# Kernel optimization log

Measured on AMD Instinct MI355X. Metric: run time of the kernel, lower is better.

The kernel has to match this reference:

```python
import jax, jax.numpy as jnp
import numpy as np

# ---- dims (match init_kwargs / input_specs) ----
N = 50000        # nodes
E = 600000       # edges
F_IN = 128       # n_features
HID = 128        # hidden_dims
K = 8            # heads
D_A = 16         # attention dim per head
D_V = 16         # value dim per head
D_M = 64         # max-pool gate dim
CLASSES = 40     # n_classes
LAYERS = 2
SLOPE = 0.1      # negative_slop


def glorot(key, shape):
    lim = jnp.sqrt(6.0 / (shape[-2] + shape[-1]))
    return jax.random.uniform(key, shape, minval=-lim, maxval=lim, dtype=jnp.float32)


def setup_inputs() -> dict:
    key = jax.random.key(0)
    ks = jax.random.split(key, 10)
    x = jax.random.normal(ks[0], (N, F_IN), dtype=jnp.float32)
    edge_index = jax.random.randint(ks[1], (2, E), 0, N, dtype=jnp.int64)
    weight_in = glorot(ks[2], (F_IN, HID))
    weight_out = glorot(ks[3], (HID, CLASSES))
    # per-layer GaANConv params, stacked on leading layer dim
    Wq = glorot(ks[4], (LAYERS, HID, K * D_A))            # query proj
    Wk = glorot(ks[5], (LAYERS, HID, K * D_A))            # key proj
    Wv = glorot(ks[6], (LAYERS, HID, K * D_V))            # value proj
    Wm = glorot(ks[7], (LAYERS, HID, D_M))                # max-pool gate proj
    Wg = glorot(ks[8], (LAYERS, HID + D_M + HID, K))      # gate FC
    Wo = glorot(ks[9], (LAYERS, HID + K * D_V, HID))      # output proj
    return {"x": x, "edge_index": edge_index, "weight_in": weight_in,
            "weight_out": weight_out, "Wq": Wq, "Wk": Wk, "Wv": Wv,
            "Wm": Wm, "Wg": Wg, "Wo": Wo}


def gaan_conv(x, src, dst, wq, wk, wv, wm, wg, wo):
    n = x.shape[0]
    q = (x @ wq).reshape(n, K, D_A)
    k = (x @ wk).reshape(n, K, D_A)
    v = (x @ wv).reshape(n, K, D_V)
    # dot-product attention logits per edge/head: <q_dst, k_src>
    score = jnp.einsum('ekd,ekd->ek', q[dst], k[src])          # [E,K]
    # segment softmax over incoming edges of each dst node
    smax = jax.ops.segment_max(score, dst, num_segments=n)     # [N,K]
    smax = jnp.where(jnp.isfinite(smax), smax, 0.0)            # empty segments -> 0
    ex = jnp.exp(score - smax[dst])
    denom = jax.ops.segment_sum(ex, dst, num_segments=n)
    alpha = ex / (denom[dst] + 1e-16)                          # [E,K]
    agg = jax.ops.segment_sum(alpha[:, :, None] * v[src], dst, num_segments=n)  # [N,K,D_V]
    # gates: sigmoid(FC([x_i, max_j FC_m(x_j), mean_j x_j]))
    m = x @ wm                                                 # [N,D_M]
    maxpool = jax.ops.segment_max(m[src], dst, num_segments=n)
    maxpool = jnp.where(jnp.isfinite(maxpool), maxpool, 0.0)
    deg = jax.ops.segment_sum(jnp.ones((src.shape[0],), x.dtype), dst, num_segments=n)
    meanpool = jax.ops.segment_sum(x[src], dst, num_segments=n) / jnp.maximum(deg, 1.0)[:, None]
    g = jax.nn.sigmoid(jnp.concatenate([x, maxpool, meanpool], axis=1) @ wg)  # [N,K]
    gated = (g[:, :, None] * agg).reshape(n, K * D_V)
    return jnp.concatenate([x, gated], axis=1) @ wo            # [N,HID]


def reference(x, edge_index, weight_in, weight_out, Wq, Wk, Wv, Wm, Wg, Wo):
    src, dst = edge_index[0], edge_index[1]
    h = x @ weight_in
    for i in range(LAYERS):
        h = jax.nn.leaky_relu(
            gaan_conv(h, src, dst, Wq[i], Wk[i], Wv[i], Wm[i], Wg[i], Wo[i]),
            negative_slope=SLOPE)
        # dropout is identity in eval mode
    out = h @ weight_out
    return jax.nn.log_softmax(out, axis=1)
```

## Files before the change

kernel.cpp:

```cpp
#include <hip/hip_runtime.h>
#include <math.h>

#define NNODES 50000
#define NEDGES 600000
#define HIDDIM 128
#define NHEAD 8
#define DM 64
#define NCLS 40
#define FSTR 584
#define OFF_K 128
#define OFF_V 256
#define OFF_M 384
#define OFF_HG 448
#define OFF_H 456

typedef __attribute__((ext_vector_type(8))) short short8;
typedef __attribute__((ext_vector_type(4))) float f32x4;

static __device__ __forceinline__ unsigned short f2bf(float f) {
    unsigned u = __float_as_uint(f);
    unsigned r = (u + 0x7fffu + ((u >> 16) & 1u)) >> 16;
    return (unsigned short)r;
}
static __device__ __forceinline__ float bflo(unsigned u) { return __uint_as_float(u << 16); }
static __device__ __forceinline__ float bfhi(unsigned u) { return __uint_as_float(u & 0xffff0000u); }
static __device__ __forceinline__ float bf2f(unsigned short s) {
    return __uint_as_float(((unsigned)s) << 16);
}

template <int WF32, int WB1, int ACT>
__global__ __launch_bounds__(256) void gemm_mfma(
    const unsigned short* __restrict__ A1, int lda1, int K1,
    const unsigned short* __restrict__ A2, int lda2, int K2,
    const unsigned short* __restrict__ BT,
    float* __restrict__ C, int ldc,
    unsigned short* __restrict__ Cb1, int ldb1, int off1,
    int M, int NN)
{
    const int K = K1 + K2;
    const int l = threadIdx.x & 63, wv = threadIdx.x >> 6;
    const int r = l & 15, g = l >> 4;
    const int row0 = blockIdx.y * 128 + wv * 32;
    const int col0 = blockIdx.x * 64;

    f32x4 acc[2][4] = {};

    for (int k0 = 0; k0 < K; k0 += 32) {
        const unsigned short* Ak;
        int ka, lda;
        if (k0 < K1) { Ak = A1; ka = k0; lda = lda1; }
        else         { Ak = A2; ka = k0 - K1; lda = lda2; }

        short8 a[2], b[4];
#pragma unroll
        for (int m = 0; m < 2; ++m) {
            int row = row0 + m * 16 + r;
            if (row < M)
                a[m] = *reinterpret_cast<const short8*>(Ak + (size_t)row * lda + ka + 8 * g);
            else
                a[m] = short8{0, 0, 0, 0, 0, 0, 0, 0};
        }
#pragma unroll
        for (int n = 0; n < 4; ++n) {
            int col = col0 + n * 16 + r;
            b[n] = *reinterpret_cast<const short8*>(BT + (size_t)col * K + k0 + 8 * g);
        }
#pragma unroll
        for (int m = 0; m < 2; ++m)
#pragma unroll
            for (int n = 0; n < 4; ++n)
                acc[m][n] = __builtin_amdgcn_mfma_f32_16x16x32_bf16(a[m], b[n], acc[m][n], 0, 0, 0);
    }

#pragma unroll
    for (int m = 0; m < 2; ++m) {
#pragma unroll
        for (int j = 0; j < 4; ++j) {
            int row = row0 + m * 16 + 4 * g + j;
            if (row >= M) continue;
#pragma unroll
            for (int n = 0; n < 4; ++n) {
                int col = col0 + n * 16 + r;
                if (col >= NN) continue;
                float vv = acc[m][n][j];
                if (ACT) vv = vv > 0.f ? vv : 0.1f * vv;
                if (WF32) C[(size_t)row * ldc + col] = vv;
                if (WB1)  Cb1[(size_t)row * ldb1 + off1 + col] = f2bf(vv);
            }
        }
    }
}

#define BT_TOTAL 206848
__global__ __launch_bounds__(256) void pack_weights(
    const float* __restrict__ w_in, const float* __restrict__ w_out,
    const float* __restrict__ Wq, const float* __restrict__ Wk,
    const float* __restrict__ Wv, const float* __restrict__ Wm,
    const float* __restrict__ Wg, const float* __restrict__ Wo,
    unsigned short* __restrict__ BT)
{
    int i = blockIdx.x * 256 + threadIdx.x;
    if (i >= BT_TOTAL) return;
    float val;
    if (i < 16384) {
        int c = i >> 7, k = i & 127;
        val = w_in[k * 128 + c];
    } else if (i < 133120) {
        int li = i - 16384;
        int L = li / 58368, t = li % 58368;
        int c = t >> 7, k = t & 127;
        if      (c < 128) val = Wq[L * 16384 + k * 128 + c];
        else if (c < 256) val = Wk[L * 16384 + k * 128 + (c - 128)];
        else if (c < 384) val = Wv[L * 16384 + k * 128 + (c - 256)];
        else if (c < 448) val = Wm[L * 8192  + k * 64  + (c - 384)];
        else              val = Wg[L * 2560 + (192 + k) * 8 + (c - 448)];
    } else if (i < 198656) {
        int li = i - 133120;
        int L = li / 32768, t = li % 32768;
        int c = t >> 8, k = t & 255;
        val = Wo[L * 32768 + k * 128 + c];
    } else {
        int t = i - 198656;
        int c = t >> 7, k = t & 127;
        val = (c < NCLS) ? w_out[k * NCLS + c] : 0.f;
    }
    BT[i] = f2bf(val);
}

__global__ __launch_bounds__(256) void convert_x_kernel(
    const float* __restrict__ x, unsigned int* __restrict__ xb2)
{
    int i = blockIdx.x * 256 + threadIdx.x;
    if (i >= NNODES * HIDDIM / 2) return;
    float2 f = *reinterpret_cast<const float2*>(x + (size_t)i * 2);
    xb2[i] = (unsigned)f2bf(f.x) | ((unsigned)f2bf(f.y) << 16);
}

__global__ __launch_bounds__(256) void hist_kernel(
    const int* __restrict__ ei, int* __restrict__ degi)
{
    int e = blockIdx.x * 256 + threadIdx.x;
    if (e >= NEDGES) return;
    unsigned d = (unsigned)ei[NEDGES + e]; if (d >= NNODES) d = 0;
    atomicAdd(&degi[d], 1);
}

__global__ __launch_bounds__(1024) void scan_kernel(
    const int* __restrict__ degi, int* __restrict__ rowptr)
{
    __shared__ int sh[1024];
    const int t = threadIdx.x;
    const int chunk = (NNODES + 1023) / 1024;
    int lo = t * chunk, hi = min(lo + chunk, NNODES);
    int s = 0;
    for (int i = lo; i < hi; ++i) s += degi[i];
    sh[t] = s;
    __syncthreads();
    for (int off = 1; off < 1024; off <<= 1) {
        int v = (t >= off) ? sh[t - off] : 0;
        __syncthreads();
        sh[t] += v;
        __syncthreads();
    }
    int excl = (t == 0) ? 0 : sh[t - 1];
    for (int i = lo; i < hi; ++i) {
        rowptr[i] = excl;
        excl += degi[i];
    }
    if (t == 1023) rowptr[NNODES] = excl;
}

__global__ __launch_bounds__(256) void scatter_kernel(
    const int* __restrict__ ei, const int* __restrict__ rowptr,
    int* __restrict__ fill, int* __restrict__ csr_src)
{
    int e = blockIdx.x * 256 + threadIdx.x;
    if (e >= NEDGES) return;
    unsigned s = (unsigned)ei[e];          if (s >= NNODES) s = 0;
    unsigned d = (unsigned)ei[NEDGES + e]; if (d >= NNODES) d = 0;
    int pos = rowptr[d] + atomicAdd(&fill[d], 1);
    csr_src[pos] = (int)s;
}

__global__ __launch_bounds__(256) void fused_edge_kernel(
    const int* __restrict__ rowptr, const int* __restrict__ csr_src,
    const unsigned short* __restrict__ feat, const float* __restrict__ Wg,
    unsigned short* __restrict__ gatedb)
{
    int node = blockIdx.x * 4 + (threadIdx.x >> 6);
    if (node >= NNODES) return;
    const int lane = threadIdx.x & 63;
    const int c2 = lane * 2;
    const int j0 = lane & 7;

    const int start = rowptr[node], end = rowptr[node + 1];
    const int deg = end - start;

    const unsigned short* frow = feat + (size_t)node * FSTR;
    unsigned qu = *reinterpret_cast<const unsigned*>(frow + c2);
    float qx = bflo(qu), qy = bfhi(qu);

    float mr = -INFINITY, dr = 0.f;
    float a0 = 0.f, a1 = 0.f;
    float hgs = 0.f;
    float mm = -INFINITY;

    int p = start;
    for (; p + 2 <= end; p += 2) {
        int s0 = csr_src[p], s1 = csr_src[p + 1];
        const unsigned short* r0 = feat + (size_t)s0 * FSTR;
        const unsigned short* r1 = feat + (size_t)s1 * FSTR;
        unsigned ku0 = *reinterpret_cast<const unsigned*>(r0 + OFF_K + c2);
        unsigned vu0 = *reinterpret_cast<const unsigned*>(r0 + OFF_V + c2);
        float    mv0 = bf2f(r0[OFF_M + lane]);
        float    hg0 = bf2f(r0[OFF_HG + j0]);
        unsigned ku1 = *reinterpret_cast<const unsigned*>(r1 + OFF_K + c2);
        unsigned vu1 = *reinterpret_cast<const unsigned*>(r1 + OFF_V + c2);
        float    mv1 = bf2f(r1[OFF_M + lane]);
        float    hg1 = bf2f(r1[OFF_HG + j0]);

        float sc0 = qx * bflo(ku0) + qy * bfhi(ku0);
        float sc1 = qx * bflo(ku1) + qy * bfhi(ku1);
        sc0 += __shfl_xor(sc0, 1);  sc1 += __shfl_xor(sc1, 1);
        sc0 += __shfl_xor(sc0, 2);  sc1 += __shfl_xor(sc1, 2);
        sc0 += __shfl_xor(sc0, 4);  sc1 += __shfl_xor(sc1, 4);

        float nm = fmaxf(mr, fmaxf(sc0, sc1));
        float scale = __expf(mr - nm);
        float e0 = __expf(sc0 - nm), e1 = __expf(sc1 - nm);
        dr = dr * scale + e0 + e1;
        a0 = a0 * scale; a0 = fmaf(e0, bflo(vu0), a0); a0 = fmaf(e1, bflo(vu1), a0);
        a1 = a1 * scale; a1 = fmaf(e0, bfhi(vu0), a1); a1 = fmaf(e1, bfhi(vu1), a1);
        mr = nm;

        hgs += hg0 + hg1;
        mm = fmaxf(mm, fmaxf(mv0, mv1));
    }
    if (p < end) {
        int s0 = csr_src[p];
        const unsigned short* r0 = feat + (size_t)s0 * FSTR;
        unsigned ku0 = *reinterpret_cast<const unsigned*>(r0 + OFF_K + c2);
        unsigned vu0 = *reinterpret_cast<const unsigned*>(r0 + OFF_V + c2);
        float    mv0 = bf2f(r0[OFF_M + lane]);
        float    hg0 = bf2f(r0[OFF_HG + j0]);

        float sc0 = qx * bflo(ku0) + qy * bfhi(ku0);
        sc0 += __shfl_xor(sc0, 1);
        sc0 += __shfl_xor(sc0, 2);
        sc0 += __shfl_xor(sc0, 4);

        float nm = fmaxf(mr, sc0);
        float scale = __expf(mr - nm);
        float e0 = __expf(sc0 - nm);
        dr = dr * scale + e0;
        a0 = fmaf(e0, bflo(vu0), a0 * scale);
        a1 = fmaf(e0, bfhi(vu0), a1 * scale);
        mr = nm;

        hgs += hg0;
        mm = fmaxf(mm, mv0);
    }

    float inv  = 1.f / (dr + 1e-16f);
    float invd = 1.f / fmaxf((float)deg, 1.f);
    if (deg == 0) { mm = 0.f; inv = 0.f; }

    unsigned hou = *reinterpret_cast<const unsigned*>(frow + OFF_H + c2);
    float hx = bflo(hou), hy = bfhi(hou);

    const float* w0 = Wg + (size_t)c2 * 8;
    const float* w1 = Wg + (size_t)(c2 + 1) * 8;
    const float* w2 = Wg + (size_t)(128 + lane) * 8;

    float part[8];
#pragma unroll
    for (int j = 0; j < 8; ++j)
        part[j] = hx * w0[j] + hy * w1[j] + mm * w2[j];
#pragma unroll
    for (int off = 1; off < 64; off <<= 1)
#pragma unroll
        for (int j = 0; j < 8; ++j)
            part[j] += __shfl_xor(part[j], off);

    float mc = __shfl(hgs, lane >> 3);
    float gg = 1.f / (1.f + __expf(-(part[lane >> 3] + mc * invd)));
    float o0 = gg * a0 * inv, o1 = gg * a1 * inv;
    unsigned outu = (unsigned)f2bf(o0) | ((unsigned)f2bf(o1) << 16);
    *reinterpret_cast<unsigned*>(gatedb + (size_t)node * HIDDIM + c2) = outu;
}

__global__ __launch_bounds__(256) void logsoftmax_kernel(float* __restrict__ out)
{
    int gt = blockIdx.x * 256 + threadIdx.x;
    int wid = gt >> 6;
    int lane = threadIdx.x & 63;
    if (wid >= NNODES) return;
    float* row = out + (size_t)wid * NCLS;
    float x = (lane < NCLS) ? row[lane] : -INFINITY;
    float mx = x;
#pragma unroll
    for (int off = 32; off; off >>= 1) mx = fmaxf(mx, __shfl_xor(mx, off));
    float ex = (lane < NCLS) ? __expf(x - mx) : 0.f;
    float sm = ex;
#pragma unroll
    for (int off = 32; off; off >>= 1) sm += __shfl_xor(sm, off);
    float lse = mx + logf(sm);
    if (lane < NCLS) row[lane] = x - lse;
}

static inline int cdiv(int a, int b) { return (a + b - 1) / b; }

extern "C" void kernel_launch(void* const* d_in, const int* in_sizes, int n_in,
                              void* d_out, int out_size, void* d_ws, size_t ws_size,
                              hipStream_t stream)
{
    const float* x     = (const float*)d_in[0];
    const int*   ei    = (const int*)d_in[1];
    const float* w_in  = (const float*)d_in[2];
    const float* w_out = (const float*)d_in[3];
    const float* Wq    = (const float*)d_in[4];
    const float* Wk    = (const float*)d_in[5];
    const float* Wv    = (const float*)d_in[6];
    const float* Wm    = (const float*)d_in[7];
    const float* Wg    = (const float*)d_in[8];
    const float* Wo    = (const float*)d_in[9];
    float* out = (float*)d_out;

    const size_t NF = NNODES;
    unsigned short* xb     = (unsigned short*)d_ws;
    unsigned short* feat0  = xb    + NF * 128;
    unsigned short* feat1  = feat0 + NF * FSTR;
    unsigned short* gatedb = feat1 + NF * FSTR;
    unsigned short* BTpool = gatedb + NF * 128;
    int* rowptr  = (int*)(BTpool + BT_TOTAL);
    int* degi    = rowptr + (NNODES + 1);
    int* fill    = degi + NNODES;
    int* csr_src = fill + NNODES;

    const unsigned short* BTin    = BTpool;
    const unsigned short* BTqkvm0 = BTpool + 16384;
    const unsigned short* BTqkvm1 = BTpool + 74752;
    const unsigned short* BTo0    = BTpool + 133120;
    const unsigned short* BTo1    = BTpool + 165888;
    const unsigned short* BTout   = BTpool + 198656;

    pack_weights<<<cdiv(BT_TOTAL, 256), 256, 0, stream>>>(
        w_in, w_out, Wq, Wk, Wv, Wm, Wg, Wo, BTpool);
    convert_x_kernel<<<cdiv(NNODES * HIDDIM / 2, 256), 256, 0, stream>>>(
        x, (unsigned int*)xb);
    hipMemsetAsync(degi, 0, 2 * NNODES * sizeof(int), stream);
    hist_kernel<<<cdiv(NEDGES, 256), 256, 0, stream>>>(ei, degi);
    scan_kernel<<<1, 1024, 0, stream>>>(degi, rowptr);
    scatter_kernel<<<cdiv(NEDGES, 256), 256, 0, stream>>>(ei, rowptr, fill, csr_src);

    const dim3 g128(2, cdiv(NNODES, 128));
    const dim3 g456(8, cdiv(NNODES, 128));
    const dim3 g40 (1, cdiv(NNODES, 128));

    gemm_mfma<0, 1, 0><<<g128, 256, 0, stream>>>(
        xb, 128, 128, nullptr, 0, 0, BTin,
        nullptr, 0, feat0, FSTR, OFF_H, NNODES, 128);

    unsigned short* featA = feat0;
    unsigned short* featB = feat1;
    for (int L = 0; L < 2; ++L) {
        const unsigned short* btq = L ? BTqkvm1 : BTqkvm0;
        const unsigned short* bto = L ? BTo1 : BTo0;
        const float* wg = Wg + (size_t)L * 320 * 8;

        gemm_mfma<0, 1, 0><<<g456, 256, 0, stream>>>(
            featA + OFF_H, FSTR, 128, nullptr, 0, 0, btq,
            nullptr, 0, featA, FSTR, 0, NNODES, 456);

        fused_edge_kernel<<<cdiv(NNODES, 4), 256, 0, stream>>>(
            rowptr, csr_src, featA, wg, gatedb);

        gemm_mfma<0, 1, 1><<<g128, 256, 0, stream>>>(
            featA + OFF_H, FSTR, 128, gatedb, 128, 128, bto,
            nullptr, 0, featB, FSTR, OFF_H, NNODES, 128);

        unsigned short* t = featA; featA = featB; featB = t;
    }

    gemm_mfma<1, 0, 0><<<g40, 256, 0, stream>>>(
        featA + OFF_H, FSTR, 128, nullptr, 0, 0, BTout,
        out, NCLS, nullptr, 0, 0, NNODES, NCLS);
    logsoftmax_kernel<<<cdiv(NNODES * 64, 256), 256, 0, stream>>>(out);
}
```

Measured before the change: 556.5 us.

## Parallelize CSR prefix scan across blocks and enlarge GEMM row tiles

```diff
diff --git a/kernel.cpp b/kernel.cpp
--- a/kernel.cpp
+++ b/kernel.cpp
@@ -13,6 +13,7 @@
 #define OFF_M 384
 #define OFF_HG 448
 #define OFF_H 456
+#define NBLK 196
 
 typedef __attribute__((ext_vector_type(8))) short short8;
 typedef __attribute__((ext_vector_type(4))) float f32x4;
@@ -40,10 +41,10 @@
     const int K = K1 + K2;
     const int l = threadIdx.x & 63, wv = threadIdx.x >> 6;
     const int r = l & 15, g = l >> 4;
-    const int row0 = blockIdx.y * 128 + wv * 32;
+    const int row0 = blockIdx.y * 256 + wv * 64;
     const int col0 = blockIdx.x * 64;
 
-    f32x4 acc[2][4] = {};
+    f32x4 acc[4][4] = {};
 
     for (int k0 = 0; k0 < K; k0 += 32) {
         const unsigned short* Ak;
@@ -51,9 +52,9 @@
         if (k0 < K1) { Ak = A1; ka = k0; lda = lda1; }
         else         { Ak = A2; ka = k0 - K1; lda = lda2; }
 
-        short8 a[2], b[4];
-#pragma unroll
-        for (int m = 0; m < 2; ++m) {
+        short8 a[4], b[4];
+#pragma unroll
+        for (int m = 0; m < 4; ++m) {
             int row = row0 + m * 16 + r;
             if (row < M)
                 a[m] = *reinterpret_cast<const short8*>(Ak + (size_t)row * lda + ka + 8 * g);
@@ -66,14 +67,14 @@
             b[n] = *reinterpret_cast<const short8*>(BT + (size_t)col * K + k0 + 8 * g);
         }
 #pragma unroll
-        for (int m = 0; m < 2; ++m)
+        for (int m = 0; m < 4; ++m)
 #pragma unroll
             for (int n = 0; n < 4; ++n)
                 acc[m][n] = __builtin_amdgcn_mfma_f32_16x16x32_bf16(a[m], b[n], acc[m][n], 0, 0, 0);
     }
 
 #pragma unroll
-    for (int m = 0; m < 2; ++m) {
+    for (int m = 0; m < 4; ++m) {
 #pragma unroll
         for (int j = 0; j < 4; ++j) {
             int row = row0 + m * 16 + 4 * g + j;
@@ -145,29 +146,57 @@
     atomicAdd(&degi[d], 1);
 }
 
-__global__ __launch_bounds__(1024) void scan_kernel(
-    const int* __restrict__ degi, int* __restrict__ rowptr)
-{
-    __shared__ int sh[1024];
+static __device__ __forceinline__ int wave_incl_scan(int x, int lane) {
+#pragma unroll
+    for (int off = 1; off < 64; off <<= 1) {
+        int n = __shfl_up(x, off);
+        if (lane >= off) x += n;
+    }
+    return x;
+}
+
+__global__ __launch_bounds__(256) void scan_blk_kernel(
+    const int* __restrict__ degi, int* __restrict__ rowptr,
+    int* __restrict__ bsum)
+{
+    __shared__ int wsum[4];
+    const int t = threadIdx.x, b = blockIdx.x;
+    const int idx = b * 256 + t;
+    const int lane = t & 63, wv = t >> 6;
+    int v = (idx < NNODES) ? degi[idx] : 0;
+    int incl = wave_incl_scan(v, lane);
+    if (lane == 63) wsum[wv] = incl;
+    __syncthreads();
+    int wpre = 0;
+#pragma unroll
+    for (int w = 0; w < 4; ++w) wpre += (w < wv) ? wsum[w] : 0;
+    if (idx < NNODES) rowptr[idx] = wpre + incl - v;
+    if (t == 255) bsum[b] = wpre + incl;
+}
+
+__global__ __launch_bounds__(256) void scan_top_kernel(
+    const int* __restrict__ bsum, int* __restrict__ boff,
+    int* __restrict__ rowptr)
+{
+    __shared__ int wsum[4];
     const int t = threadIdx.x;
-    const int chunk = (NNODES + 1023) / 1024;
-    int lo = t * chunk, hi = min(lo + chunk, NNODES);
-    int s = 0;
-    for (int i = lo; i < hi; ++i) s += degi[i];
-    sh[t] = s;
+    const int lane = t & 63, wv = t >> 6;
+    int v = (t < NBLK) ? bsum[t] : 0;
+    int incl = wave_incl_scan(v, lane);
+    if (lane == 63) wsum[wv] = incl;
     __syncthreads();
-    for (int off = 1; off < 1024; off <<= 1) {
-        int v = (t >= off) ? sh[t - off] : 0;
-        __syncthreads();
-        sh[t] += v;
-        __syncthreads();
-    }
-    int excl = (t == 0) ? 0 : sh[t - 1];
-    for (int i = lo; i < hi; ++i) {
-        rowptr[i] = excl;
-        excl += degi[i];
-    }
-    if (t == 1023) rowptr[NNODES] = excl;
+    int wpre = 0;
+#pragma unroll
+    for (int w = 0; w < 4; ++w) wpre += (w < wv) ? wsum[w] : 0;
+    if (t < NBLK) boff[t] = wpre + incl - v;
+    if (t == 0) rowptr[NNODES] = NEDGES;
+}
+
+__global__ __launch_bounds__(256) void scan_add_kernel(
+    int* __restrict__ rowptr, const int* __restrict__ boff)
+{
+    int idx = blockIdx.x * 256 + threadIdx.x;
+    if (idx < NNODES) rowptr[idx] += boff[blockIdx.x];
 }
 
 __global__ __launch_bounds__(256) void scatter_kernel(
@@ -336,6 +365,8 @@
     int* degi    = rowptr + (NNODES + 1);
     int* fill    = degi + NNODES;
     int* csr_src = fill + NNODES;
+    int* bsum    = csr_src + NEDGES;
+    int* boff    = bsum + NBLK;
 
     const unsigned short* BTin    = BTpool;
     const unsigned short* BTqkvm0 = BTpool + 16384;
@@ -350,12 +381,14 @@
         x, (unsigned int*)xb);
     hipMemsetAsync(degi, 0, 2 * NNODES * sizeof(int), stream);
     hist_kernel<<<cdiv(NEDGES, 256), 256, 0, stream>>>(ei, degi);
-    scan_kernel<<<1, 1024, 0, stream>>>(degi, rowptr);
+    scan_blk_kernel<<<NBLK, 256, 0, stream>>>(degi, rowptr, bsum);
+    scan_top_kernel<<<1, 256, 0, stream>>>(bsum, boff, rowptr);
+    scan_add_kernel<<<NBLK, 256, 0, stream>>>(rowptr, boff);
     scatter_kernel<<<cdiv(NEDGES, 256), 256, 0, stream>>>(ei, rowptr, fill, csr_src);
 
-    const dim3 g128(2, cdiv(NNODES, 128));
-    const dim3 g456(8, cdiv(NNODES, 128));
-    const dim3 g40 (1, cdiv(NNODES, 128));
+    const dim3 g128(2, cdiv(NNODES, 256));
+    const dim3 g456(8, cdiv(NNODES, 256));
+    const dim3 g40 (1, cdiv(NNODES, 256));
 
     gemm_mfma<0, 1, 0><<<g128, 256, 0, stream>>>(
         xb, 128, 128, nullptr, 0, 0, BTin,
```

Result: faster. 475.3 us (-14.6%).
